# Performance work log

Hardware: AMD Instinct MI355X
Metric: run time of the kernel (lower is better)

Reference implementation:

```python
import jax, jax.numpy as jnp
import numpy as np

B, H, W, C, HEADS, SR = 4, 64, 64, 256, 8, 2
D = C // HEADS            # head dim = 32
SCALE = D ** -0.5
EPS = 1e-6


def _conv(x, w, stride, pad, groups):
    return jax.lax.conv_general_dilated(
        x, w, (stride, stride), [(pad, pad), (pad, pad)],
        feature_group_count=groups,
        dimension_numbers=('NCHW', 'OIHW', 'NCHW'))


def setup_inputs() -> dict:
    key = jax.random.key(0)
    ks = jax.random.split(key, 9)
    s = lambda fan: 1.0 / np.sqrt(fan)
    return {
        'x': jax.random.normal(ks[0], (B, H * W, C), jnp.float32),
        'dw_w': jax.random.normal(ks[1], (C, 1, 3, 3), jnp.float32) * s(9),
        'dw_b': jnp.zeros((C,), jnp.float32),
        'pw_w': jax.random.normal(ks[2], (C, C, 1, 1), jnp.float32) * s(C),
        'pw_b': jnp.zeros((C,), jnp.float32),
        'sr_w': jax.random.normal(ks[3], (C, 1, 3, 3), jnp.float32) * s(9),
        'ln_g': jnp.ones((C,), jnp.float32),
        'ln_b': jnp.zeros((C,), jnp.float32),
        'kv_w': jax.random.normal(ks[4], (2 * C, C), jnp.float32) * s(C),
        'kv_b': jnp.zeros((2 * C,), jnp.float32),
        'proj_w': jax.random.normal(ks[5], (C, C), jnp.float32) * s(C),
        'proj_b': jnp.zeros((C,), jnp.float32),
    }


def reference(x, dw_w, dw_b, pw_w, pw_b, sr_w, ln_g, ln_b, kv_w, kv_b, proj_w, proj_b):
    Bx, N, Cx = x.shape
    # Q path: depthwise-separable conv on the spatial layout
    xq = x.reshape(Bx, H, W, Cx).transpose(0, 3, 1, 2)          # (B,C,H,W)
    q = _conv(xq, dw_w, 1, 1, Cx) + dw_b[None, :, None, None]    # depthwise 3x3
    q = _conv(q, pw_w, 1, 0, 1) + pw_b[None, :, None, None]      # pointwise 1x1
    # 'b (h d) l w -> b h (l w) d'
    q = q.reshape(Bx, HEADS, D, H * W).transpose(0, 1, 3, 2)     # (B,h,N,d)

    # SR path for K/V: strided depthwise conv + LayerNorm
    x_ = _conv(xq, sr_w, SR, SR // 2, Cx)                        # (B,C,H/SR,W/SR)
    x_ = x_.reshape(Bx, Cx, -1).transpose(0, 2, 1)               # (B,M,C)
    mu = jnp.mean(x_, axis=-1, keepdims=True)
    var = jnp.mean(jnp.square(x_ - mu), axis=-1, keepdims=True)
    x_ = (x_ - mu) * jax.lax.rsqrt(var + EPS) * ln_g + ln_b

    kv = x_ @ kv_w.T + kv_b                                      # (B,M,2C)
    M = kv.shape[1]
    kv = kv.reshape(Bx, M, 2, HEADS, D).transpose(2, 0, 3, 1, 4) # (2,B,h,M,d)
    k, v = kv[0], kv[1]

    attn = jnp.einsum('bhnd,bhmd->bhnm', q, k) * SCALE           # (B,h,N,M)
    attn = jax.nn.softmax(attn, axis=-1)
    out = jnp.einsum('bhnm,bhmd->bhnd', attn, v)                 # (B,h,N,d)
    out = out.transpose(0, 2, 1, 3).reshape(Bx, N, Cx)           # (B,N,C)
    return out @ proj_w.T + proj_b
```

## Files before the change

### kernel.cpp

```cpp
#include <hip/hip_runtime.h>
#include <math.h>

#define BB 4
#define HH 64
#define WW 64
#define CC 256
#define NN 4096
#define MM 1024
#define LN_EPS 1e-6f
#define SLF (0.17677669529663687f * 1.4426950408889634f)

typedef __attribute__((ext_vector_type(8)))  short short8;
typedef __attribute__((ext_vector_type(16))) float f32x16;

__device__ __forceinline__ ushort f2bf(float f) {
  unsigned u = __builtin_bit_cast(unsigned, f);
  u += 0x7fffu + ((u >> 16) & 1u);
  return (ushort)(u >> 16);
}
__device__ __forceinline__ float bf2f(ushort h) {
  unsigned u = ((unsigned)h) << 16;
  return __builtin_bit_cast(float, u);
}
#if __has_builtin(__builtin_amdgcn_exp2f)
#define EXP2F(x) __builtin_amdgcn_exp2f(x)
#else
#define EXP2F(x) exp2f(x)
#endif

__global__ __launch_bounds__(256) void pre_fused(
    const float* __restrict__ x, const float* __restrict__ dw_w,
    const float* __restrict__ dw_b, const float* __restrict__ sr_w,
    const float* __restrict__ ln_g, const float* __restrict__ ln_b,
    const float* __restrict__ pw_w, const float* __restrict__ kv_w,
    const float* __restrict__ proj_w,
    ushort* __restrict__ q1b, ushort* __restrict__ xsr,
    ushort* __restrict__ pwB, ushort* __restrict__ kvB,
    ushort* __restrict__ pjH, ushort* __restrict__ pjL) {
  int bid = blockIdx.x;
  int c = threadIdx.x;
  if (bid < 4096) {
    int b = bid >> 10, m = bid & 1023;
    int my = m >> 5, mx = m & 31;
    const float* xb = x + (size_t)b * NN * CC + c;
    float acc = 0.f;
#pragma unroll
    for (int dy = 0; dy < 3; ++dy) {
      int iy = 2 * my + dy - 1;
      if (iy < 0 || iy >= HH) continue;
#pragma unroll
      for (int dx = 0; dx < 3; ++dx) {
        int ix = 2 * mx + dx - 1;
        if (ix < 0 || ix >= WW) continue;
        acc += xb[(size_t)(iy * WW + ix) * CC] * sr_w[c * 9 + dy * 3 + dx];
      }
    }
    float v1 = acc, v2 = acc * acc;
#pragma unroll
    for (int s = 1; s < 64; s <<= 1) {
      v1 += __shfl_xor(v1, s);
      v2 += __shfl_xor(v2, s);
    }
    __shared__ float r1[4], r2[4];
    int lane = c & 63, wv = c >> 6;
    if (lane == 0) { r1[wv] = v1; r2[wv] = v2; }
    __syncthreads();
    float s1 = r1[0] + r1[1] + r1[2] + r1[3];
    float s2 = r2[0] + r2[1] + r2[2] + r2[3];
    float mu = s1 * (1.f / 256.f);
    float var = s2 * (1.f / 256.f) - mu * mu;
    float yv = (acc - mu) * rsqrtf(var + LN_EPS) * ln_g[c] + ln_b[c];
    xsr[((size_t)b * MM + m) * CC + c] = f2bf(yv);
  } else if (bid < 4608) {
    int id = bid - 4096;
    int b = id >> 7, yy = id & 127;
    int y = yy >> 1, hf = yy & 1;
    float wr[9];
#pragma unroll
    for (int i = 0; i < 9; ++i) wr[i] = dw_w[c * 9 + i];
    float bi = dw_b[c];
    const float* xb = x + (size_t)b * NN * CC + c;
    int x0 = hf * 32;
    bool okT = (y > 0), okB = (y < 63);
    float a0, a1, a2, b0, b1, b2;
    if (x0 == 0) {
      a0 = a1 = a2 = 0.f;
    } else {
      a0 = okT ? xb[(size_t)((y - 1) * 64 + x0 - 1) * CC] : 0.f;
      a1 = xb[(size_t)(y * 64 + x0 - 1) * CC];
      a2 = okB ? xb[(size_t)((y + 1) * 64 + x0 - 1) * CC] : 0.f;
    }
    b0 = okT ? xb[(size_t)((y - 1) * 64 + x0) * CC] : 0.f;
    b1 = xb[(size_t)(y * 64 + x0) * CC];
    b2 = okB ? xb[(size_t)((y + 1) * 64 + x0) * CC] : 0.f;
    ushort* ob = q1b + ((size_t)b * NN + y * 64) * CC + c;
#pragma unroll 8
    for (int xx = x0; xx < x0 + 32; ++xx) {
      float c0v, c1v, c2v;
      if (xx < 63) {
        c0v = okT ? xb[(size_t)((y - 1) * 64 + xx + 1) * CC] : 0.f;
        c1v = xb[(size_t)(y * 64 + xx + 1) * CC];
        c2v = okB ? xb[(size_t)((y + 1) * 64 + xx + 1) * CC] : 0.f;
      } else {
        c0v = c1v = c2v = 0.f;
      }
      float acc = bi;
      acc += a0 * wr[0] + b0 * wr[1] + c0v * wr[2];
      acc += a1 * wr[3] + b1 * wr[4] + c1v * wr[5];
      acc += a2 * wr[6] + b2 * wr[7] + c2v * wr[8];
      ob[(size_t)xx * CC] = f2bf(acc);
      a0 = b0; a1 = b1; a2 = b2;
      b0 = c0v; b1 = c1v; b2 = c2v;
    }
  } else if (bid < 4672) {
    int i0 = (bid - 4608) * 1024 + c * 4;
    float4 v = *(const float4*)&pw_w[i0];
    ushort tmp[4] = {f2bf(v.x), f2bf(v.y), f2bf(v.z), f2bf(v.w)};
    *(uint2*)&pwB[i0] = *(uint2*)tmp;
  } else if (bid < 4800) {
    int i0 = (bid - 4672) * 1024 + c * 4;
    float4 v = *(const float4*)&kv_w[i0];
    ushort tmp[4] = {f2bf(v.x), f2bf(v.y), f2bf(v.z), f2bf(v.w)};
    *(uint2*)&kvB[i0] = *(uint2*)tmp;
  } else {
    int i0 = (bid - 4800) * 1024 + c * 4;
    float4 v = *(const float4*)&proj_w[i0];
    float vv[4] = {v.x, v.y, v.z, v.w};
    ushort th[4], tl[4];
#pragma unroll
    for (int j = 0; j < 4; ++j) {
      th[j] = f2bf(vv[j]);
      tl[j] = f2bf(vv[j] - bf2f(th[j]));
    }
    *(uint2*)&pjH[i0] = *(uint2*)th;
    *(uint2*)&pjL[i0] = *(uint2*)tl;
  }
}

__global__ __launch_bounds__(256) void gemm_qkv(
    const ushort* __restrict__ q1b, const ushort* __restrict__ xsr,
    const ushort* __restrict__ pwB, const float* __restrict__ pw_b,
    const ushort* __restrict__ kvB, const float* __restrict__ kv_b,
    ushort* __restrict__ qB, ushort* __restrict__ kB,
    ushort* __restrict__ vT) {
  __shared__ ushort smem[2][128 * 40];
  int bid = blockIdx.x;
  bool is0 = bid < 1024;
  const ushort* A;
  const ushort* W;
  const float* bias;
  int r0, c0;
  if (is0) {
    A = q1b; W = pwB; bias = pw_b;
    r0 = (bid >> 2) * 64; c0 = (bid & 3) * 64;
  } else {
    int sid = bid - 1024;
    A = xsr; W = kvB; bias = kv_b;
    r0 = (sid >> 3) * 64; c0 = (sid & 7) * 64;
  }
  const bool vmode = (!is0) && (c0 >= 256);

  int t = threadIdx.x;
  int lane = t & 63, w = t >> 6;
  int l31 = lane & 31, half = lane >> 5;
  int wr = w >> 1, wc = w & 1;
  int rowA = t >> 2, kq = (t & 3) * 8;

  f32x16 acc;
#pragma unroll
  for (int i = 0; i < 16; ++i) acc[i] = 0.f;

  short8 ra, rw;
  auto prefetch = [&](int kc) {
    ra = *(const short8*)&A[(size_t)(r0 + rowA) * 256 + kc + kq];
    rw = *(const short8*)&W[(size_t)(c0 + rowA) * 256 + kc + kq];
  };
  auto store = [&](ushort* buf) {
    *(short8*)&buf[rowA * 40 + kq] = ra;
    *(short8*)&buf[64 * 40 + rowA * 40 + kq] = rw;
  };

  prefetch(0);
  store(smem[0]);
  __syncthreads();
  for (int i = 0; i < 8; ++i) {
    ushort* cur = smem[i & 1];
    ushort* nxt = smem[(i & 1) ^ 1];
    if (i < 7) prefetch((i + 1) * 32);
#pragma unroll
    for (int ks = 0; ks < 2; ++ks) {
      short8 af = *(const short8*)&cur[(wr * 32 + l31) * 40 + ks * 16 + half * 8];
      short8 wf = *(const short8*)&cur[64 * 40 + (wc * 32 + l31) * 40 + ks * 16 + half * 8];
      if (vmode)
        acc = __builtin_amdgcn_mfma_f32_32x32x16_bf16(wf, af, acc, 0, 0, 0);
      else
        acc = __builtin_amdgcn_mfma_f32_32x32x16_bf16(af, wf, acc, 0, 0, 0);
    }
    if (i < 7) store(nxt);
    __syncthreads();
  }

#pragma unroll
  for (int i = 0; i < 16; ++i) {
    int rl = (i & 3) + 8 * (i >> 2) + 4 * half;
    if (is0) {
      int r = r0 + wr * 32 + rl;
      int c = c0 + wc * 32 + l31;
      int b = r >> 12, n = r & 4095;
      int h = c >> 5, d = c & 31;
      qB[((size_t)(b * 8 + h) * NN + n) * 32 + d] =
          f2bf((acc[i] + bias[c]) * SLF);
    } else if (!vmode) {
      int r = r0 + wr * 32 + rl;
      int c = c0 + wc * 32 + l31;
      int b = r >> 10, m = r & 1023;
      int h = c >> 5, d = c & 31;
      kB[((size_t)(b * 8 + h) * MM + m) * 32 + d] = f2bf(acc[i] + bias[c]);
    } else {
      int c = c0 + wc * 32 + rl;
      int r = r0 + wr * 32 + l31;
      int b = r >> 10, m = r & 1023;
      int cv = c - 256;
      int h = cv >> 5, d = cv & 31;
      vT[((size_t)(b * 8 + h) * 32 + d) * MM + m] = f2bf(acc[i] + bias[c]);
    }
  }
}

__global__ __launch_bounds__(256, 4) void attn_mfma(
    const ushort* __restrict__ qB, const ushort* __restrict__ kB,
    const ushort* __restrict__ vT, ushort* __restrict__ aH,
    ushort* __restrict__ aL) {
  __shared__ ushort sKa[2][8][264];
  __shared__ ushort sVa[2][8][264];
  __shared__ ushort pB[4][4][512];
  int t = threadIdx.x;
  int lane = t & 63, w = t >> 6;
  int l31 = lane & 31, half = lane >> 5;
  int bh = blockIdx.x;
  int b = bh >> 3, h = bh & 7;
  int q0 = blockIdx.y * 128;

  const ushort* qrow = qB + ((size_t)bh * NN + q0 + w * 32 + l31) * 32;
  short8 bq0 = *(const short8*)(qrow + half * 8);
  short8 bq1 = *(const short8*)(qrow + 16 + half * 8);

  const ushort* kbase = kB + (size_t)bh * MM * 32;
  const ushort* vbase = vT + (size_t)bh * 32 * MM;
  int krow = t >> 2, kq = (t & 3) * 8;
  int vd = t >> 3, vmo = (t & 7) * 8;
  int kreg_idx = (krow >> 5) * 4 + (kq >> 4) * 2 + ((kq >> 3) & 1);
  int klane = (krow & 31) * 8;
  int vreg_idx = (vmo >> 4) * 2 + ((vmo >> 3) & 1);
  int vlane = vd * 8;

  short8 kreg = *(const short8*)&kbase[(size_t)krow * 32 + kq];
  short8 vreg = *(const short8*)&vbase[(size_t)vd * MM + vmo];
  *(short8*)&sKa[0][kreg_idx][klane] = kreg;
  *(short8*)&sVa[0][vreg_idx][vlane] = vreg;

  f32x16 o;
#pragma unroll
  for (int i = 0; i < 16; ++i) o[i] = 0.f;
  float psum = 0.f;
  __syncthreads();

  for (int mc = 0; mc < 16; ++mc) {
    int cur = mc & 1, nxt = cur ^ 1;
    if (mc < 15) {
      int m0n = (mc + 1) * 64;
      kreg = *(const short8*)&kbase[(size_t)(m0n + krow) * 32 + kq];
      vreg = *(const short8*)&vbase[(size_t)vd * MM + m0n + vmo];
    }
    f32x16 st[2];
    __builtin_amdgcn_s_setprio(1);
#pragma unroll
    for (int tt = 0; tt < 2; ++tt) {
      short8 a0 = *(const short8*)&sKa[cur][tt * 4 + 0 + half][l31 * 8];
      short8 a1 = *(const short8*)&sKa[cur][tt * 4 + 2 + half][l31 * 8];
      f32x16 z;
#pragma unroll
      for (int i = 0; i < 16; ++i) z[i] = 0.f;
      z = __builtin_amdgcn_mfma_f32_32x32x16_bf16(a0, bq0, z, 0, 0, 0);
      z = __builtin_amdgcn_mfma_f32_32x32x16_bf16(a1, bq1, z, 0, 0, 0);
      st[tt] = z;
    }
    __builtin_amdgcn_s_setprio(0);

    if (mc < 15) {
      *(short8*)&sKa[nxt][kreg_idx][klane] = kreg;
      *(short8*)&sVa[nxt][vreg_idx][vlane] = vreg;
    }

#pragma unroll
    for (int tt = 0; tt < 2; ++tt) {
#pragma unroll
      for (int rg = 0; rg < 4; ++rg) {
        float p0 = EXP2F(st[tt][rg * 4 + 0]);
        float p1 = EXP2F(st[tt][rg * 4 + 1]);
        float p2 = EXP2F(st[tt][rg * 4 + 2]);
        float p3 = EXP2F(st[tt][rg * 4 + 3]);
        psum += (p0 + p1) + (p2 + p3);
        uint2 pk;
        pk.x = __builtin_amdgcn_perm(__builtin_bit_cast(unsigned, p1),
                                     __builtin_bit_cast(unsigned, p0), 0x07060302);
        pk.y = __builtin_amdgcn_perm(__builtin_bit_cast(unsigned, p3),
                                     __builtin_bit_cast(unsigned, p2), 0x07060302);
        *(uint2*)&pB[w][2 * tt + (rg >> 1)][((rg & 1) * 32 + l31) * 8 + 4 * half] = pk;
      }
    }

    __builtin_amdgcn_s_setprio(1);
#pragma unroll
    for (int kb = 0; kb < 4; ++kb) {
      short8 av = *(const short8*)&sVa[cur][kb * 2 + half][l31 * 8];
      short8 bp = *(const short8*)&pB[w][kb][lane * 8];
      o = __builtin_amdgcn_mfma_f32_32x32x16_bf16(av, bp, o, 0, 0, 0);
    }
    __builtin_amdgcn_s_setprio(0);

    __syncthreads();
  }

  float denom = psum + __shfl_xor(psum, 32);
  float inv = 1.f / denom;
  size_t rbase = ((size_t)b * NN + q0 + w * 32 + l31) * 256 + h * 32;
#pragma unroll
  for (int rg = 0; rg < 4; ++rg) {
#pragma unroll
    for (int j = 0; j < 4; ++j) {
      float v = o[rg * 4 + j] * inv;
      ushort hi = f2bf(v);
      ushort lo = f2bf(v - bf2f(hi));
      int d = rg * 8 + half * 4 + j;
      aH[rbase + d] = hi;
      aL[rbase + d] = lo;
    }
  }
}

__global__ __launch_bounds__(256) void gemm_proj(
    const ushort* __restrict__ A, const ushort* __restrict__ A2,
    const ushort* __restrict__ Whi, const ushort* __restrict__ Wlo,
    const float* __restrict__ bias, float* __restrict__ out) {
  __shared__ ushort smem[2][4 * 64 * 40];
  constexpr int OA = 0, OA2 = 64 * 40, OW = 2 * 64 * 40, OW2 = 3 * 64 * 40;
  int bid = blockIdx.x;
  int r0 = (bid >> 2) * 64, c0 = (bid & 3) * 64;

  int t = threadIdx.x;
  int lane = t & 63, w = t >> 6;
  int l31 = lane & 31, half = lane >> 5;
  int wr = w >> 1, wc = w & 1;
  int rowA = t >> 2, kq = (t & 3) * 8;

  f32x16 acc;
#pragma unroll
  for (int i = 0; i < 16; ++i) acc[i] = 0.f;

  short8 ra, ra2, rwh, rwl;
  auto prefetch = [&](int kc) {
    ra  = *(const short8*)&A[(size_t)(r0 + rowA) * 256 + kc + kq];
    ra2 = *(const short8*)&A2[(size_t)(r0 + rowA) * 256 + kc + kq];
    rwh = *(const short8*)&Whi[(size_t)(c0 + rowA) * 256 + kc + kq];
    rwl = *(const short8*)&Wlo[(size_t)(c0 + rowA) * 256 + kc + kq];
  };
  auto store = [&](ushort* buf) {
    *(short8*)&buf[OA + rowA * 40 + kq] = ra;
    *(short8*)&buf[OA2 + rowA * 40 + kq] = ra2;
    *(short8*)&buf[OW + rowA * 40 + kq] = rwh;
    *(short8*)&buf[OW2 + rowA * 40 + kq] = rwl;
  };

  prefetch(0);
  store(smem[0]);
  __syncthreads();
  for (int i = 0; i < 8; ++i) {
    ushort* cur = smem[i & 1];
    ushort* nxt = smem[(i & 1) ^ 1];
    if (i < 7) prefetch((i + 1) * 32);
#pragma unroll
    for (int ks = 0; ks < 2; ++ks) {
      int ro = (wr * 32 + l31) * 40 + ks * 16 + half * 8;
      int co = (wc * 32 + l31) * 40 + ks * 16 + half * 8;
      short8 af = *(const short8*)&cur[OA + ro];
      short8 af2 = *(const short8*)&cur[OA2 + ro];
      short8 wf = *(const short8*)&cur[OW + co];
      short8 wf2 = *(const short8*)&cur[OW2 + co];
      acc = __builtin_amdgcn_mfma_f32_32x32x16_bf16(af, wf, acc, 0, 0, 0);
      acc = __builtin_amdgcn_mfma_f32_32x32x16_bf16(af2, wf, acc, 0, 0, 0);
      acc = __builtin_amdgcn_mfma_f32_32x32x16_bf16(af, wf2, acc, 0, 0, 0);
    }
    if (i < 7) store(nxt);
    __syncthreads();
  }

#pragma unroll
  for (int i = 0; i < 16; ++i) {
    int rl = (i & 3) + 8 * (i >> 2) + 4 * half;
    int r = r0 + wr * 32 + rl;
    int c = c0 + wc * 32 + l31;
    out[(size_t)r * 256 + c] = acc[i] + bias[c];
  }
}

extern "C" void kernel_launch(void* const* d_in, const int* in_sizes, int n_in,
                              void* d_out, int out_size, void* d_ws, size_t ws_size,
                              hipStream_t stream) {
  const float* x      = (const float*)d_in[0];
  const float* dw_w   = (const float*)d_in[1];
  const float* dw_b   = (const float*)d_in[2];
  const float* pw_w   = (const float*)d_in[3];
  const float* pw_b   = (const float*)d_in[4];
  const float* sr_w   = (const float*)d_in[5];
  const float* ln_g   = (const float*)d_in[6];
  const float* ln_b   = (const float*)d_in[7];
  const float* kv_w   = (const float*)d_in[8];
  const float* kv_b   = (const float*)d_in[9];
  const float* proj_w = (const float*)d_in[10];
  const float* proj_b = (const float*)d_in[11];
  float* out = (float*)d_out;

  char* ws = (char*)d_ws;
  ushort* q1b = (ushort*)(ws);
  ushort* xsr = (ushort*)(ws + (8u << 20));
  ushort* qB  = (ushort*)(ws + (16u << 20));
  ushort* kBp = (ushort*)(ws + (24u << 20));
  ushort* vTp = (ushort*)(ws + (26u << 20));
  ushort* aH  = (ushort*)(ws + (28u << 20));
  ushort* aL  = (ushort*)(ws + (36u << 20));
  ushort* pwB = (ushort*)(ws + (44u << 20));
  ushort* kvB = (ushort*)(ws + (44u << 20) + (512u << 10));
  ushort* pjH = (ushort*)(ws + (45u << 20));
  ushort* pjL = (ushort*)(ws + (45u << 20) + (512u << 10));

  pre_fused<<<dim3(4864), 256, 0, stream>>>(x, dw_w, dw_b, sr_w, ln_g, ln_b,
                                            pw_w, kv_w, proj_w,
                                            q1b, xsr, pwB, kvB, pjH, pjL);
  gemm_qkv<<<dim3(1536), 256, 0, stream>>>(q1b, xsr, pwB, pw_b, kvB, kv_b,
                                           qB, kBp, vTp);
  attn_mfma<<<dim3(32, 32), 256, 0, stream>>>(qB, kBp, vTp, aH, aL);
  gemm_proj<<<dim3(1024), 256, 0, stream>>>(aH, aL, pjH, pjL, proj_b, out);
}
```

Measured before the change: 164.3 us.

## Deepen global-load prefetch to two stages and split depthwise conv into more blocks

The GEMM and attention kernels now keep two register stages of global loads in flight. The next tile is written to shared memory before the current MMA step, and the loads for two tiles ahead are issued at the same point, which gives load latency more time to hide behind compute. The depthwise-conv part of the preprocessing kernel now has each block handle 8 output columns instead of 32, quadrupling its block count to raise parallelism. The cost is more live registers, which may reduce occupancy, and more halo reloads in the conv.

```diff
diff --git a/kernel.cpp b/kernel.cpp
--- a/kernel.cpp
+++ b/kernel.cpp
@@ -71,16 +71,16 @@
     float var = s2 * (1.f / 256.f) - mu * mu;
     float yv = (acc - mu) * rsqrtf(var + LN_EPS) * ln_g[c] + ln_b[c];
     xsr[((size_t)b * MM + m) * CC + c] = f2bf(yv);
-  } else if (bid < 4608) {
+  } else if (bid < 6144) {
     int id = bid - 4096;
-    int b = id >> 7, yy = id & 127;
-    int y = yy >> 1, hf = yy & 1;
+    int b = id >> 9, r = id & 511;
+    int y = r >> 3, seg = r & 7;
+    int x0 = seg * 8;
     float wr[9];
 #pragma unroll
     for (int i = 0; i < 9; ++i) wr[i] = dw_w[c * 9 + i];
     float bi = dw_b[c];
     const float* xb = x + (size_t)b * NN * CC + c;
-    int x0 = hf * 32;
     bool okT = (y > 0), okB = (y < 63);
     float a0, a1, a2, b0, b1, b2;
     if (x0 == 0) {
@@ -95,7 +95,7 @@
     b2 = okB ? xb[(size_t)((y + 1) * 64 + x0) * CC] : 0.f;
     ushort* ob = q1b + ((size_t)b * NN + y * 64) * CC + c;
 #pragma unroll 8
-    for (int xx = x0; xx < x0 + 32; ++xx) {
+    for (int xx = x0; xx < x0 + 8; ++xx) {
       float c0v, c1v, c2v;
       if (xx < 63) {
         c0v = okT ? xb[(size_t)((y - 1) * 64 + xx + 1) * CC] : 0.f;
@@ -112,18 +112,18 @@
       a0 = b0; a1 = b1; a2 = b2;
       b0 = c0v; b1 = c1v; b2 = c2v;
     }
-  } else if (bid < 4672) {
-    int i0 = (bid - 4608) * 1024 + c * 4;
+  } else if (bid < 6208) {
+    int i0 = (bid - 6144) * 1024 + c * 4;
     float4 v = *(const float4*)&pw_w[i0];
     ushort tmp[4] = {f2bf(v.x), f2bf(v.y), f2bf(v.z), f2bf(v.w)};
     *(uint2*)&pwB[i0] = *(uint2*)tmp;
-  } else if (bid < 4800) {
-    int i0 = (bid - 4672) * 1024 + c * 4;
+  } else if (bid < 6336) {
+    int i0 = (bid - 6208) * 1024 + c * 4;
     float4 v = *(const float4*)&kv_w[i0];
     ushort tmp[4] = {f2bf(v.x), f2bf(v.y), f2bf(v.z), f2bf(v.w)};
     *(uint2*)&kvB[i0] = *(uint2*)tmp;
   } else {
-    int i0 = (bid - 4800) * 1024 + c * 4;
+    int i0 = (bid - 6336) * 1024 + c * 4;
     float4 v = *(const float4*)&proj_w[i0];
     float vv[4] = {v.x, v.y, v.z, v.w};
     ushort th[4], tl[4];
@@ -170,23 +170,26 @@
 #pragma unroll
   for (int i = 0; i < 16; ++i) acc[i] = 0.f;
 
-  short8 ra, rw;
-  auto prefetch = [&](int kc) {
-    ra = *(const short8*)&A[(size_t)(r0 + rowA) * 256 + kc + kq];
-    rw = *(const short8*)&W[(size_t)(c0 + rowA) * 256 + kc + kq];
+  short8 ra[2], rw[2];
+  auto prefetch = [&](int kc, int s) {
+    ra[s] = *(const short8*)&A[(size_t)(r0 + rowA) * 256 + kc + kq];
+    rw[s] = *(const short8*)&W[(size_t)(c0 + rowA) * 256 + kc + kq];
   };
-  auto store = [&](ushort* buf) {
-    *(short8*)&buf[rowA * 40 + kq] = ra;
-    *(short8*)&buf[64 * 40 + rowA * 40 + kq] = rw;
+  auto store = [&](ushort* buf, int s) {
+    *(short8*)&buf[rowA * 40 + kq] = ra[s];
+    *(short8*)&buf[64 * 40 + rowA * 40 + kq] = rw[s];
   };
 
-  prefetch(0);
-  store(smem[0]);
+  prefetch(0, 0);
+  store(smem[0], 0);
+  prefetch(32, 1);
   __syncthreads();
+#pragma unroll
   for (int i = 0; i < 8; ++i) {
     ushort* cur = smem[i & 1];
     ushort* nxt = smem[(i & 1) ^ 1];
-    if (i < 7) prefetch((i + 1) * 32);
+    if (i < 7) store(nxt, (i + 1) & 1);
+    if (i < 6) prefetch((i + 2) * 32, i & 1);
 #pragma unroll
     for (int ks = 0; ks < 2; ++ks) {
       short8 af = *(const short8*)&cur[(wr * 32 + l31) * 40 + ks * 16 + half * 8];
@@ -196,7 +199,6 @@
       else
         acc = __builtin_amdgcn_mfma_f32_32x32x16_bf16(af, wf, acc, 0, 0, 0);
     }
-    if (i < 7) store(nxt);
     __syncthreads();
   }
 
@@ -254,10 +256,13 @@
   int vreg_idx = (vmo >> 4) * 2 + ((vmo >> 3) & 1);
   int vlane = vd * 8;
 
-  short8 kreg = *(const short8*)&kbase[(size_t)krow * 32 + kq];
-  short8 vreg = *(const short8*)&vbase[(size_t)vd * MM + vmo];
-  *(short8*)&sKa[0][kreg_idx][klane] = kreg;
-  *(short8*)&sVa[0][vreg_idx][vlane] = vreg;
+  short8 kr[2], vr[2];
+  kr[0] = *(const short8*)&kbase[(size_t)krow * 32 + kq];
+  vr[0] = *(const short8*)&vbase[(size_t)vd * MM + vmo];
+  kr[1] = *(const short8*)&kbase[(size_t)(64 + krow) * 32 + kq];
+  vr[1] = *(const short8*)&vbase[(size_t)vd * MM + 64 + vmo];
+  *(short8*)&sKa[0][kreg_idx][klane] = kr[0];
+  *(short8*)&sVa[0][vreg_idx][vlane] = vr[0];
 
   f32x16 o;
 #pragma unroll
@@ -265,13 +270,10 @@
   float psum = 0.f;
   __syncthreads();
 
+#pragma unroll 2
   for (int mc = 0; mc < 16; ++mc) {
     int cur = mc & 1, nxt = cur ^ 1;
-    if (mc < 15) {
-      int m0n = (mc + 1) * 64;
-      kreg = *(const short8*)&kbase[(size_t)(m0n + krow) * 32 + kq];
-      vreg = *(const short8*)&vbase[(size_t)vd * MM + m0n + vmo];
-    }
+
     f32x16 st[2];
     __builtin_amdgcn_s_setprio(1);
 #pragma unroll
@@ -288,8 +290,13 @@
     __builtin_amdgcn_s_setprio(0);
 
     if (mc < 15) {
-      *(short8*)&sKa[nxt][kreg_idx][klane] = kreg;
-      *(short8*)&sVa[nxt][vreg_idx][vlane] = vreg;
+      *(short8*)&sKa[nxt][kreg_idx][klane] = kr[nxt];
+      *(short8*)&sVa[nxt][vreg_idx][vlane] = vr[nxt];
+    }
+    if (mc < 14) {
+      int m2 = (mc + 2) * 64;
+      kr[cur] = *(const short8*)&kbase[(size_t)(m2 + krow) * 32 + kq];
+      vr[cur] = *(const short8*)&vbase[(size_t)vd * MM + m2 + vmo];
     }
 
 #pragma unroll
@@ -358,27 +365,30 @@
 #pragma unroll
   for (int i = 0; i < 16; ++i) acc[i] = 0.f;
 
-  short8 ra, ra2, rwh, rwl;
-  auto prefetch = [&](int kc) {
-    ra  = *(const short8*)&A[(size_t)(r0 + rowA) * 256 + kc + kq];
-    ra2 = *(const short8*)&A2[(size_t)(r0 + rowA) * 256 + kc + kq];
-    rwh = *(const short8*)&Whi[(size_t)(c0 + rowA) * 256 + kc + kq];
-    rwl = *(const short8*)&Wlo[(size_t)(c0 + rowA) * 256 + kc + kq];
+  short8 ra[2], ra2[2], rwh[2], rwl[2];
+  auto prefetch = [&](int kc, int s) {
+    ra[s]  = *(const short8*)&A[(size_t)(r0 + rowA) * 256 + kc + kq];
+    ra2[s] = *(const short8*)&A2[(size_t)(r0 + rowA) * 256 + kc + kq];
+    rwh[s] = *(const short8*)&Whi[(size_t)(c0 + rowA) * 256 + kc + kq];
+    rwl[s] = *(const short8*)&Wlo[(size_t)(c0 + rowA) * 256 + kc + kq];
   };
-  auto store = [&](ushort* buf) {
-    *(short8*)&buf[OA + rowA * 40 + kq] = ra;
-    *(short8*)&buf[OA2 + rowA * 40 + kq] = ra2;
-    *(short8*)&buf[OW + rowA * 40 + kq] = rwh;
-    *(short8*)&buf[OW2 + rowA * 40 + kq] = rwl;
+  auto store = [&](ushort* buf, int s) {
+    *(short8*)&buf[OA + rowA * 40 + kq] = ra[s];
+    *(short8*)&buf[OA2 + rowA * 40 + kq] = ra2[s];
+    *(short8*)&buf[OW + rowA * 40 + kq] = rwh[s];
+    *(short8*)&buf[OW2 + rowA * 40 + kq] = rwl[s];
   };
 
-  prefetch(0);
-  store(smem[0]);
+  prefetch(0, 0);
+  store(smem[0], 0);
+  prefetch(32, 1);
   __syncthreads();
+#pragma unroll
   for (int i = 0; i < 8; ++i) {
     ushort* cur = smem[i & 1];
     ushort* nxt = smem[(i & 1) ^ 1];
-    if (i < 7) prefetch((i + 1) * 32);
+    if (i < 7) store(nxt, (i + 1) & 1);
+    if (i < 6) prefetch((i + 2) * 32, i & 1);
 #pragma unroll
     for (int ks = 0; ks < 2; ++ks) {
       int ro = (wr * 32 + l31) * 40 + ks * 16 + half * 8;
@@ -391,7 +401,6 @@
       acc = __builtin_amdgcn_mfma_f32_32x32x16_bf16(af2, wf, acc, 0, 0, 0);
       acc = __builtin_amdgcn_mfma_f32_32x32x16_bf16(af, wf2, acc, 0, 0, 0);
     }
-    if (i < 7) store(nxt);
     __syncthreads();
   }
 
@@ -434,7 +443,7 @@
   ushort* pjH = (ushort*)(ws + (45u << 20));
   ushort* pjL = (ushort*)(ws + (45u << 20) + (512u << 10));
 
-  pre_fused<<<dim3(4864), 256, 0, stream>>>(x, dw_w, dw_b, sr_w, ln_g, ln_b,
+  pre_fused<<<dim3(6400), 256, 0, stream>>>(x, dw_w, dw_b, sr_w, ln_g, ln_b,
                                             pw_w, kv_w, proj_w,
                                             q1b, xsr, pwB, kvB, pjH, pjL);
   gemm_qkv<<<dim3(1536), 256, 0, stream>>>(q1b, xsr, pwB, pw_b, kvB, kv_b,
```

Measured after the change: 155.0 us. 1.06x faster.
